# Kernel tuning notes

Hardware: AMD Instinct MI355X
Metric: run time of the kernel (lower is better)

## Reference

```python
import jax, jax.numpy as jnp
import numpy as np

DIM = 172
MULT = 4
HEADS = 1
B, H, W = 2, 256, 256


def _ln(x, g, b):
    # LayerNorm over last dim, eps=1e-5 (torch default)
    m = jnp.mean(x, axis=-1, keepdims=True)
    v = jnp.mean((x - m) ** 2, axis=-1, keepdims=True)
    return (x - m) * jax.lax.rsqrt(v + 1e-5) * g + b


def _l2norm(x):
    # F.normalize(p=2, dim=-1): x / max(||x||, 1e-12)
    n = jnp.sqrt(jnp.sum(x * x, axis=-1, keepdims=True))
    return x / jnp.maximum(n, 1e-12)


def _gelu(x):
    return jax.nn.gelu(x, approximate=False)


def _dwconv3(x, w):
    # x: [B,C,H,W], w: [C,1,3,3], groups=C, padding=1
    return jax.lax.conv_general_dilated(
        x, w, window_strides=(1, 1), padding='SAME',
        feature_group_count=x.shape[1],
        dimension_numbers=('NCHW', 'OIHW', 'NCHW'))


def _c1x1(x, w):
    # 1x1 conv, no bias. x: [B,I,H,W], w: [O,I,1,1]
    return jnp.einsum('bihw,oi->bohw', x, w[:, :, 0, 0])


def _ms_msa(x, Wq, Wk, Wv, rescale, proj_w, proj_b, pos_w1, pos_w2):
    # x: [b,h,w,c] (already layer-normed)
    b, h, w, c = x.shape
    d = c // HEADS
    n = h * w
    xf = x.reshape(b, n, c)
    q_inp = xf @ Wq.T
    k_inp = xf @ Wk.T
    v_inp = xf @ Wv.T

    def split(t):  # -> [b, heads, d, n]  (b n (h d) -> b h n d, then transpose(-2,-1))
        return t.reshape(b, n, HEADS, d).transpose(0, 2, 3, 1)

    q, k, v = split(q_inp), split(k_inp), split(v_inp)
    q = _l2norm(q)
    k = _l2norm(k)
    attn = jnp.einsum('bhdn,bhen->bhde', k, q)  # k @ q^T -> [b,heads,d,d]
    attn = attn * rescale                        # learnable per-head rescale
    attn = jax.nn.softmax(attn, axis=-1)
    xo = jnp.einsum('bhde,bhen->bhdn', attn, v)  # [b,heads,d,n]
    xo = xo.transpose(0, 3, 1, 2).reshape(b, n, HEADS * d)
    out_c = (xo @ proj_w.T + proj_b).reshape(b, h, w, c)
    # residual positional embedding: depthwise conv -> GELU -> depthwise conv on v_inp
    vim = v_inp.reshape(b, h, w, c).transpose(0, 3, 1, 2)
    out_p = _dwconv3(_gelu(_dwconv3(vim, pos_w1)), pos_w2).transpose(0, 2, 3, 1)
    return out_c + out_p


def _ffn(x, w1, dw, w2):
    # FeedForward: 1x1 expand -> GELU -> 3x3 depthwise -> GELU -> 1x1 project
    y = x.transpose(0, 3, 1, 2)
    y = _gelu(_c1x1(y, w1))
    y = _gelu(_dwconv3(y, dw))
    y = _c1x1(y, w2)
    return y.transpose(0, 2, 3, 1)


def reference(x, ln1_g, ln1_b, Wq, Wk, Wv, rescale, proj_w, proj_b,
              pos_w1, pos_w2, ln2_g, ln2_b, ff_w1, ff_dw, ff_w2):
    # SMSAB forward, num_blocks=1. x: [b,c,h,w]
    y = x.transpose(0, 2, 3, 1)  # [b,h,w,c]
    y = _ms_msa(_ln(y, ln1_g, ln1_b), Wq, Wk, Wv, rescale,
                proj_w, proj_b, pos_w1, pos_w2) + y
    y = _ffn(_ln(y, ln2_g, ln2_b), ff_w1, ff_dw, ff_w2) + y
    return y.transpose(0, 3, 1, 2)  # [b,c,h,w]


def setup_inputs() -> dict:
    key = jax.random.key(0)
    ks = jax.random.split(key, 9)
    s = 0.02
    c, m = DIM, DIM * MULT
    return {
        'x': jax.random.normal(ks[0], (B, c, H, W), jnp.float32),
        'ln1_g': jnp.ones((c,), jnp.float32),
        'ln1_b': jnp.zeros((c,), jnp.float32),
        'Wq': jax.random.normal(ks[1], (c, c), jnp.float32) * s,
        'Wk': jax.random.normal(ks[2], (c, c), jnp.float32) * s,
        'Wv': jax.random.normal(ks[3], (c, c), jnp.float32) * s,
        'rescale': jnp.ones((HEADS, 1, 1), jnp.float32),
        'proj_w': jax.random.normal(ks[4], (c, c), jnp.float32) * s,
        'proj_b': jnp.zeros((c,), jnp.float32),
        'pos_w1': jax.random.normal(ks[5], (c, 1, 3, 3), jnp.float32) * s,
        'pos_w2': jax.random.normal(ks[6], (c, 1, 3, 3), jnp.float32) * s,
        'ln2_g': jnp.ones((c,), jnp.float32),
        'ln2_b': jnp.zeros((c,), jnp.float32),
        'ff_w1': jax.random.normal(ks[7], (m, c, 1, 1), jnp.float32) * s,
        'ff_dw': jax.random.normal(ks[8], (m, 1, 3, 3), jnp.float32) * s,
        'ff_w2': jax.random.normal(jax.random.fold_in(key, 99), (c, m, 1, 1), jnp.float32) * s,
    }
```

## Files before the change

kernel.cpp:

```cpp
#include <hip/hip_runtime.h>
#include <hip/hip_bf16.h>
#include <hip/hip_fp16.h>

#define NPIX 65536
#define CP 176
#define EP 704
#define HCC 32

typedef long long i64;
typedef __attribute__((ext_vector_type(8))) short bf8v;
typedef __attribute__((ext_vector_type(8))) float f8v;
typedef __attribute__((ext_vector_type(4))) float f4v;

__device__ __forceinline__ float b2f(unsigned short u) {
  return __uint_as_float(((unsigned)u) << 16);
}
__device__ __forceinline__ short f2b(float v) {
  __hip_bfloat16 h = __float2bfloat16(v);
  return *reinterpret_cast<short*>(&h);
}
__device__ __forceinline__ float ldf(const void* p, i64 i, int bf) {
  return bf ? b2f(((const unsigned short*)p)[i]) : ((const float*)p)[i];
}
__device__ __forceinline__ float gelu_f(float x) {
  return x / (1.f + __expf(-1.702f * x));
}
__device__ __forceinline__ bf8v ldbf8(const short* p) { return *(const bf8v*)p; }

__global__ void detect_k(const void* g, int* flag) {
  unsigned u = *(const unsigned*)g;
  *flag = (u == 0x3F800000u) ? 0 : 1;
}

__global__ __launch_bounds__(256) void prep_k(
    const void* Wv, const void* fw1, const void* fw2, const void* Wq,
    const void* posw1, const void* posw2, const void* fdw,
    const void* pb, const void* ln2g, const void* ln2b,
    short* Wvb, short* fw1b, short* fw2b, float* Wqt,
    float* p1f, float* p2f, float* fdwf, float* pbf, float* gf, float* bfv,
    float* Gf, const int* flagp)
{
  const int flag = *flagp;
  const int bx = blockIdx.x, t = threadIdx.x;
  switch (blockIdx.y) {
    case 0: {
      if (t < 176) Wvb[(i64)bx * 176 + t] =
        f2b((bx < 172 && t < 172) ? ldf(Wv, (i64)bx * 172 + t, flag) : 0.f);
    } break;
    case 1: {
      if (t < 176)
        for (int m = bx; m < 704; m += 176)
          fw1b[(i64)m * 176 + t] =
            f2b((m < 688 && t < 172) ? ldf(fw1, (i64)m * 172 + t, flag) : 0.f);
    } break;
    case 2: {
      for (int k = t; k < 704; k += 256)
        fw2b[(i64)bx * 704 + k] =
          f2b((bx < 172 && k < 688) ? ldf(fw2, (i64)bx * 688 + k, flag) : 0.f);
    } break;
    case 3: {
      if (t < 176) Wqt[(i64)bx * 176 + t] =
        (bx < 172 && t < 172) ? ldf(Wq, (i64)t * 172 + bx, flag) : 0.f;
    } break;
    case 4: {
      if (bx < 9 && t < 176) p1f[bx * 176 + t] = (t < 172) ? ldf(posw1, (i64)t * 9 + bx, flag) : 0.f;
    } break;
    case 5: {
      if (bx < 9 && t < 176) p2f[bx * 176 + t] = (t < 172) ? ldf(posw2, (i64)t * 9 + bx, flag) : 0.f;
    } break;
    case 6: {
      if (bx < 9)
        for (int c = t; c < 704; c += 256)
          fdwf[bx * 704 + c] = (c < 688) ? ldf(fdw, (i64)c * 9 + bx, flag) : 0.f;
    } break;
    case 7: {
      if (bx == 0 && t < 176) {
        pbf[t] = (t < 172) ? ldf(pb, t, flag) : 0.f;
        gf[t]  = (t < 172) ? ldf(ln2g, t, flag) : 0.f;
        bfv[t] = (t < 172) ? ldf(ln2b, t, flag) : 0.f;
      }
    } break;
    default: {
      for (int i = bx * 256 + t; i < 2 * 176 * 176; i += 176 * 256) Gf[i] = 0.f;
    } break;
  }
}

__global__ __launch_bounds__(256) void ln1_k(const void* __restrict__ x,
    const void* __restrict__ g, const void* __restrict__ bv,
    short* __restrict__ A1, const int* __restrict__ flagp)
{
  const int flag = *flagp;
  __shared__ float gs[176], bs[176];
  __shared__ float part[64][9];
  const int tid = threadIdx.x;
  if (tid < 176) {
    gs[tid] = (tid < 172) ? ldf(g, tid, flag) : 0.f;
    bs[tid] = (tid < 172) ? ldf(bv, tid, flag) : 0.f;
  }
  const int w = tid >> 6, l = tid & 63;
  const i64 gp = (i64)blockIdx.x * 64 + l;
  const int b = (int)(gp >> 16); const i64 n = gp & 65535;
  const i64 xb = (i64)b * 172 * NPIX + n;
  const bf8v z = {0, 0, 0, 0, 0, 0, 0, 0};
  bf8v keep[6];
  float s = 0.f, s2 = 0.f;
  #pragma unroll
  for (int i = 0; i < 6; ++i) {
    int c8 = w + i * 4;
    bf8v t = z;
    if (c8 < 22) {
      #pragma unroll
      for (int j = 0; j < 8; ++j) {
        int c = c8 * 8 + j;
        float v = 0.f;
        if (c < 172) { v = ldf(x, xb + (i64)c * NPIX, flag); s += v; s2 += v * v; }
        t[j] = f2b(v);
      }
    }
    keep[i] = t;
  }
  part[l][w * 2] = s; part[l][w * 2 + 1] = s2;
  __syncthreads();
  float S  = part[l][0] + part[l][2] + part[l][4] + part[l][6];
  float S2 = part[l][1] + part[l][3] + part[l][5] + part[l][7];
  float m = S * (1.f / 172.f);
  float rstd = rsqrtf(S2 * (1.f / 172.f) - m * m + 1e-5f);
  #pragma unroll
  for (int i = 0; i < 6; ++i) {
    int c8 = w + i * 4;
    if (c8 < 22) {
      bf8v t = keep[i], o;
      #pragma unroll
      for (int j = 0; j < 8; ++j) {
        int c = c8 * 8 + j;
        float y = (c < 172) ? (b2f((unsigned short)t[j]) - m) * rstd * gs[c] + bs[c] : 0.f;
        o[j] = f2b(y);
      }
      *(bf8v*)(A1 + gp * 176 + c8 * 8) = o;
    }
  }
}

__global__ __launch_bounds__(256) void gg_k(const short* __restrict__ A1,
                                            float* __restrict__ Gf)
{
  __shared__ short tile[176 * 136];
  const int tid = threadIdx.x;
  const int w = tid >> 6, l = tid & 63, lm = l & 15, ld = l >> 4;
  const int b = blockIdx.y;
  const int row = tid & 127, h = tid >> 7;
  const bf8v z = {0, 0, 0, 0, 0, 0, 0, 0};

  f4v acc[3][11];
  #pragma unroll
  for (int i = 0; i < 3; ++i)
    #pragma unroll
    for (int f = 0; f < 11; ++f) acc[i][f] = f4v{0.f, 0.f, 0.f, 0.f};

  for (int sub = 0; sub < 4; ++sub) {
    __syncthreads();
    const i64 nbase = (i64)blockIdx.x * 512 + sub * 128;
    const short* src = A1 + ((i64)b * NPIX + nbase + row) * 176 + h * 88;
    #pragma unroll
    for (int i = 0; i < 11; ++i) {
      bf8v v = ldbf8(src + i * 8);
      int c0 = h * 88 + i * 8;
      #pragma unroll
      for (int j = 0; j < 8; ++j) tile[(c0 + j) * 136 + row] = v[j];
    }
    __syncthreads();
    #pragma unroll
    for (int ks = 0; ks < 4; ++ks) {
      const int ko = ks * 32 + ld * 8;
      bf8v av[3], bv[11];
      #pragma unroll
      for (int i = 0; i < 3; ++i) {
        int fd = w + i * 4;
        av[i] = (fd < 11) ? *(const bf8v*)&tile[(fd * 16 + lm) * 136 + ko] : z;
      }
      #pragma unroll
      for (int f = 0; f < 11; ++f)
        bv[f] = *(const bf8v*)&tile[(f * 16 + lm) * 136 + ko];
      #pragma unroll
      for (int i = 0; i < 3; ++i)
        #pragma unroll
        for (int f = 0; f < 11; ++f)
          acc[i][f] = __builtin_amdgcn_mfma_f32_16x16x32_bf16(av[i], bv[f], acc[i][f], 0, 0, 0);
    }
  }
  #pragma unroll
  for (int i = 0; i < 3; ++i) {
    int fd = w + i * 4;
    if (fd >= 11) continue;
    #pragma unroll
    for (int f = 0; f < 11; ++f)
      #pragma unroll
      for (int r = 0; r < 4; ++r) {
        int d = fd * 16 + ld * 4 + r;
        int e = f * 16 + lm;
        atomicAdd(Gf + ((i64)b * 176 + d) * 176 + e, acc[i][f][r]);
      }
  }
}

__global__ __launch_bounds__(256) void attn_k1(const float* __restrict__ Gf,
    const void* __restrict__ Wk, const void* __restrict__ Wq,
    float* __restrict__ T, float* __restrict__ invk, float* __restrict__ invq,
    const int* __restrict__ flagp)
{
  const int flag = *flagp;
  const int d = blockIdx.x, b = blockIdx.y, e = threadIdx.x;
  const float* G = Gf + (i64)b * 176 * 176;
  float t = 0.f, tq = 0.f;
  if (e < 176) {
    for (int c = 0; c < 172; ++c) {
      float g = G[(i64)c * 176 + e];
      t  += ldf(Wk, (i64)d * 172 + c, flag) * g;
      tq += ldf(Wq, (i64)d * 172 + c, flag) * g;
    }
    T[((i64)b * 176 + d) * 176 + e] = t;
  }
  float pk = (e < 172) ? t  * ldf(Wk, (i64)d * 172 + e, flag) : 0.f;
  float pq = (e < 172) ? tq * ldf(Wq, (i64)d * 172 + e, flag) : 0.f;
  __shared__ float r1[256], r2[256];
  r1[e] = pk; r2[e] = pq; __syncthreads();
  for (int st = 128; st > 0; st >>= 1) {
    if (e < st) { r1[e] += r1[e + st]; r2[e] += r2[e + st]; }
    __syncthreads();
  }
  if (e == 0) {
    invk[b * 176 + d] = 1.f / fmaxf(sqrtf(fmaxf(r1[0], 0.f)), 1e-12f);
    invq[b * 176 + d] = 1.f / fmaxf(sqrtf(fmaxf(r2[0], 0.f)), 1e-12f);
  }
}

__global__ __launch_bounds__(256) void attn_k2(const float* __restrict__ T,
    const float* __restrict__ Wqt, const float* __restrict__ invk,
    const float* __restrict__ invq, const void* __restrict__ resc,
    float* __restrict__ attnf, const int* __restrict__ flagp)
{
  const int flag = *flagp;
  const int d = blockIdx.x, b = blockIdx.y, e = threadIdx.x;
  __shared__ float tl[176];
  const float* Trow = T + ((i64)b * 176 + d) * 176;
  if (e < 176) tl[e] = Trow[e];
  __syncthreads();
  float val = -1e30f;
  if (e < 172) {
    float a = 0.f;
    for (int c = 0; c < 172; ++c) a += tl[c] * Wqt[(i64)c * 176 + e];
    val = a * invk[b * 176 + d] * invq[b * 176 + e] * ldf(resc, 0, flag);
  }
  __shared__ float red[256];
  red[e] = val; __syncthreads();
  for (int st = 128; st > 0; st >>= 1) {
    if (e < st) red[e] = fmaxf(red[e], red[e + st]);
    __syncthreads();
  }
  float mx = red[0]; __syncthreads();
  float ex = (e < 172) ? __expf(val - mx) : 0.f;
  red[e] = ex; __syncthreads();
  for (int st = 128; st > 0; st >>= 1) {
    if (e < st) red[e] += red[e + st];
    __syncthreads();
  }
  float sm = red[0];
  if (e < 176) attnf[((i64)b * 176 + d) * 176 + e] = (e < 172) ? ex / sm : 0.f;
}

__global__ __launch_bounds__(256) void attn_k3(const float* __restrict__ attnf,
    const void* __restrict__ pw, short* __restrict__ Mb, const int* __restrict__ flagp)
{
  const int flag = *flagp;
  const int o = blockIdx.x, b = blockIdx.y, e = threadIdx.x;
  if (e >= 176) return;
  float m = 0.f;
  if (o < 172 && e < 172)
    for (int d = 0; d < 172; ++d)
      m += ldf(pw, (i64)o * 172 + d, flag) * attnf[((i64)b * 176 + d) * 176 + e];
  Mb[((i64)b * CP + o) * CP + e] = f2b(m);
}

__global__ __launch_bounds__(256) void ffn1_k(
    const short* __restrict__ A1,
    const short* __restrict__ fw1b,
    const float* __restrict__ fdwf,
    short* __restrict__ F, i64 fbs,
    int y0glob)
{
  __shared__ __half ering[3][256][HCC];
  __shared__ __half2 wl[9][HCC / 2];
  const int tid = threadIdx.x;
  const int w = tid >> 6, l = tid & 63, lm = l & 15, ld = l >> 4;
  const int hc0 = blockIdx.x * HCC;
  const int b = blockIdx.z;
  const int yb0 = y0glob + blockIdx.y * 8;
  for (int i = tid; i < 9 * HCC; i += 256)
    ((__half*)wl)[i] = __float2half(fdwf[(i / HCC) * EP + hc0 + (i % HCC)]);

  const short* Wl = fw1b + (i64)(hc0 + lm) * CP + ld * 8;
  const bf8v z = {0, 0, 0, 0, 0, 0, 0, 0};

  for (int yy = yb0 - 1; yy <= yb0 + 8; ++yy) {
    const int slot = (yy - (yb0 - 1)) % 3;
    __syncthreads();
    if (yy >= 0 && yy < 256) {
      const i64 prow = (i64)b * NPIX + (i64)yy * 256;
      const short* Xbase = A1 + prow * CP;
      f4v acc[2][4];
      #pragma unroll
      for (int m = 0; m < 2; ++m)
        #pragma unroll
        for (int nt = 0; nt < 4; ++nt) acc[m][nt] = f4v{0.f, 0.f, 0.f, 0.f};
      #pragma unroll
      for (int ks = 0; ks < 6; ++ks) {
        const int ko = ks * 32;
        const bool ok = (ks < 5) || (ld < 2);
        bf8v av[4], bv[2];
        #pragma unroll
        for (int nt = 0; nt < 4; ++nt) {
          const int px0 = (w * 4 + nt) * 16;
          av[nt] = ok ? ldbf8(Xbase + (i64)(px0 + lm) * CP + ld * 8 + ko) : z;
        }
        #pragma unroll
        for (int m = 0; m < 2; ++m)
          bv[m] = ok ? ldbf8(Wl + (i64)m * 16 * CP + ko) : z;
        #pragma unroll
        for (int m = 0; m < 2; ++m)
          #pragma unroll
          for (int nt = 0; nt < 4; ++nt)
            acc[m][nt] = __builtin_amdgcn_mfma_f32_16x16x32_bf16(av[nt], bv[m], acc[m][nt], 0, 0, 0);
      }
      #pragma unroll
      for (int m = 0; m < 2; ++m)
        #pragma unroll
        for (int nt = 0; nt < 4; ++nt) {
          const int px0 = (w * 4 + nt) * 16;
          #pragma unroll
          for (int r = 0; r < 4; ++r)
            ering[slot][px0 + ld * 4 + r][m * 16 + lm] = __float2half(gelu_f(acc[m][nt][r]));
        }
    } else {
      unsigned* ep = (unsigned*)&ering[slot][0][0];
      for (int i = tid; i < 256 * HCC / 2; i += 256) ep[i] = 0u;
    }
    __syncthreads();
    const int fy = yy - 1;
    if (fy >= yb0 && fy <= yb0 + 7) {
      #pragma unroll
      for (int it = 0; it < 4; ++it) {
        const int item = tid + it * 256;
        const int px = item >> 2, g = item & 3;
        __half2 a4[4];
        #pragma unroll
        for (int j = 0; j < 4; ++j) a4[j] = __half2{__half(0.f), __half(0.f)};
        #pragma unroll
        for (int dy = -1; dy <= 1; ++dy) {
          const int sl = (fy + dy - yb0 + 1) % 3;
          #pragma unroll
          for (int dx = -1; dx <= 1; ++dx) {
            const int xx = px + dx;
            if (xx < 0 || xx > 255) continue;
            const __half2* v = (const __half2*)&ering[sl][xx][g * 8];
            const __half2* wp = &wl[(dy + 1) * 3 + (dx + 1)][g * 4];
            #pragma unroll
            for (int j = 0; j < 4; ++j) a4[j] = __hfma2(v[j], wp[j], a4[j]);
          }
        }
        bf8v o;
        #pragma unroll
        for (int j = 0; j < 4; ++j) {
          float2 f = __half22float2(a4[j]);
          o[2 * j]     = f2b(gelu_f(f.x));
          o[2 * j + 1] = f2b(gelu_f(f.y));
        }
        const i64 frow = (i64)(fy - y0glob) * 256 + px;
        *(bf8v*)(F + b * fbs + frow * (i64)EP + hc0 + g * 8) = o;
      }
    }
  }
}

template<int MODE, bool GELU_>
__global__ __launch_bounds__(256) void gemm_k(
    const short* __restrict__ Wb, i64 wbs,
    const short* __restrict__ X, i64 xbs, int Kp,
    const float* __restrict__ bias,
    const short* __restrict__ add0, i64 a0bs,
    const void* __restrict__ xres,
    void* __restrict__ outp, i64 obs, int ocols, i64 out_n0,
    short* __restrict__ Y1,
    const float* __restrict__ gf, const float* __restrict__ bfv,
    const int* __restrict__ flagp)
{
  __shared__ short tl[(MODE >= 2) ? 4 * 32 * 176 : 1];
  __shared__ float2 stt[(MODE == 3) ? 4 * 32 : 1];
  const int tid = threadIdx.x;
  const int w = tid >> 6, l = tid & 63;
  const int lm = l & 15, ld = l >> 4;
  const int b = blockIdx.z;
  const int co0 = blockIdx.y * CP;
  const i64 nloc = (i64)blockIdx.x * 128 + w * 32;

  const short* Xl = X + b * xbs + (nloc + lm) * (i64)Kp + ld * 8;
  const short* Wl = Wb + b * wbs + (i64)(co0 + lm) * Kp + ld * 8;

  f4v acc[2][11];
  #pragma unroll
  for (int a = 0; a < 2; ++a)
    #pragma unroll
    for (int f = 0; f < 11; ++f) acc[a][f] = f4v{0.f, 0.f, 0.f, 0.f};

  const int nfull = Kp >> 5;
  for (int s = 0; s < nfull; ++s) {
    const int ko = s * 32;
    bf8v av0 = ldbf8(Xl + ko);
    bf8v av1 = ldbf8(Xl + (i64)16 * Kp + ko);
    bf8v bv[11];
    #pragma unroll
    for (int f = 0; f < 11; ++f) bv[f] = ldbf8(Wl + (i64)f * 16 * Kp + ko);
    #pragma unroll
    for (int f = 0; f < 11; ++f) {
      acc[0][f] = __builtin_amdgcn_mfma_f32_16x16x32_bf16(av0, bv[f], acc[0][f], 0, 0, 0);
      acc[1][f] = __builtin_amdgcn_mfma_f32_16x16x32_bf16(av1, bv[f], acc[1][f], 0, 0, 0);
    }
  }
  if (Kp & 31) {
    const int ko = nfull * 32;
    const bf8v z = {0, 0, 0, 0, 0, 0, 0, 0};
    const bool ok = (ld < 2);
    bf8v av0 = ok ? ldbf8(Xl + ko) : z;
    bf8v av1 = ok ? ldbf8(Xl + (i64)16 * Kp + ko) : z;
    bf8v bv[11];
    #pragma unroll
    for (int f = 0; f < 11; ++f) bv[f] = ok ? ldbf8(Wl + (i64)f * 16 * Kp + ko) : z;
    #pragma unroll
    for (int f = 0; f < 11; ++f) {
      acc[0][f] = __builtin_amdgcn_mfma_f32_16x16x32_bf16(av0, bv[f], acc[0][f], 0, 0, 0);
      acc[1][f] = __builtin_amdgcn_mfma_f32_16x16x32_bf16(av1, bv[f], acc[1][f], 0, 0, 0);
    }
  }

  const int flag = (MODE >= 2) ? *flagp : 0;

  if (MODE == 0) {
    #pragma unroll
    for (int a = 0; a < 2; ++a)
      #pragma unroll
      for (int f = 0; f < 11; ++f) {
        const int col = co0 + f * 16 + lm;
        #pragma unroll
        for (int r = 0; r < 4; ++r) {
          float v = acc[a][f][r];
          if (GELU_) v = gelu_f(v);
          const i64 row = nloc + a * 16 + ld * 4 + r;
          ((short*)outp)[b * obs + row * ocols + col] = f2b(v);
        }
      }
  } else if (MODE == 2) {
    #pragma unroll
    for (int a = 0; a < 2; ++a)
      #pragma unroll
      for (int f = 0; f < 11; ++f) {
        const int col = co0 + f * 16 + lm;
        #pragma unroll
        for (int r = 0; r < 4; ++r) {
          const int row32 = a * 16 + ld * 4 + r;
          tl[(w * 32 + row32) * 176 + col] = f2b(acc[a][f][r]);
        }
      }
    #pragma unroll
    for (int cc = 0; cc < 3; ++cc) {
      const int col = l + cc * 64;
      if (col < 172) {
        const i64 gn = out_n0 + nloc;
        bf8v vv[4], yv[4];
        #pragma unroll
        for (int i = 0; i < 4; ++i)
          #pragma unroll
          for (int j = 0; j < 8; ++j)
            vv[i][j] = tl[(w * 32 + i * 8 + j) * 176 + col];
        const short* yp = Y1 + ((i64)b * CP + col) * NPIX + gn;
        #pragma unroll
        for (int i = 0; i < 4; ++i) yv[i] = ldbf8(yp + i * 8);
        if (flag) {
          short* op = (short*)outp + ((i64)b * 172 + col) * NPIX + gn;
          #pragma unroll
          for (int i = 0; i < 4; ++i) {
            bf8v ov;
            #pragma unroll
            for (int j = 0; j < 8; ++j)
              ov[j] = f2b(b2f((unsigned short)vv[i][j]) + b2f((unsigned short)yv[i][j]));
            *(bf8v*)(op + i * 8) = ov;
          }
        } else {
          float* op = (float*)outp + ((i64)b * 172 + col) * NPIX + gn;
          #pragma unroll
          for (int i = 0; i < 4; ++i) {
            f8v fo;
            #pragma unroll
            for (int j = 0; j < 8; ++j)
              fo[j] = b2f((unsigned short)vv[i][j]) + b2f((unsigned short)yv[i][j]);
            *(f8v*)(op + i * 8) = fo;
          }
        }
      }
    }
  } else {
    #pragma unroll
    for (int a = 0; a < 2; ++a)
      #pragma unroll
      for (int f = 0; f < 11; ++f) {
        const int col = co0 + f * 16 + lm;
        const float bvl = bias ? bias[col] : 0.f;
        #pragma unroll
        for (int r = 0; r < 4; ++r) {
          float v = acc[a][f][r] + bvl;
          const int row32 = a * 16 + ld * 4 + r;
          const i64 row = nloc + row32;
          v += b2f(((const unsigned short*)add0)[b * a0bs + row * ocols + col]);
          tl[(w * 32 + row32) * 176 + col] = f2b(v);
        }
      }
    #pragma unroll
    for (int cc = 0; cc < 3; ++cc) {
      const int col = l + cc * 64;
      if (col < 172) {
        bf8v vv[4];
        #pragma unroll
        for (int i = 0; i < 4; ++i)
          #pragma unroll
          for (int j = 0; j < 8; ++j)
            vv[i][j] = tl[(w * 32 + i * 8 + j) * 176 + col];
        const i64 xoff = ((i64)b * 172 + col) * NPIX + nloc;
        if (flag) {
          #pragma unroll
          for (int i = 0; i < 4; ++i) {
            bf8v xv = ldbf8((const short*)xres + xoff + i * 8);
            #pragma unroll
            for (int j = 0; j < 8; ++j)
              vv[i][j] = f2b(b2f((unsigned short)vv[i][j]) + b2f((unsigned short)xv[j]));
          }
        } else {
          const float* xp = (const float*)xres + xoff;
          #pragma unroll
          for (int i = 0; i < 4; ++i) {
            f8v xv = *(const f8v*)(xp + i * 8);
            #pragma unroll
            for (int j = 0; j < 8; ++j)
              vv[i][j] = f2b(b2f((unsigned short)vv[i][j]) + xv[j]);
          }
        }
        short* yp = Y1 + ((i64)b * CP + col) * NPIX + nloc;
        #pragma unroll
        for (int i = 0; i < 4; ++i) {
          #pragma unroll
          for (int j = 0; j < 8; ++j)
            tl[(w * 32 + i * 8 + j) * 176 + col] = vv[i][j];
          *(bf8v*)(yp + i * 8) = vv[i];
        }
      }
    }
    {
      const int p = l >> 1, h = l & 1;
      float s_ = 0.f, q_ = 0.f;
      #pragma unroll
      for (int ii = 0; ii < 11; ++ii) {
        bf8v v = *(const bf8v*)&tl[(w * 32 + p) * 176 + (h * 11 + ii) * 8];
        #pragma unroll
        for (int j = 0; j < 8; ++j) { float t = b2f((unsigned short)v[j]); s_ += t; q_ += t * t; }
      }
      s_ += __shfl_xor(s_, 1); q_ += __shfl_xor(q_, 1);
      if (h == 0) {
        float mean = s_ * (1.f / 172.f);
        float rstd = rsqrtf(q_ * (1.f / 172.f) - mean * mean + 1e-5f);
        stt[w * 32 + p] = make_float2(mean, rstd);
      }
    }
    #pragma unroll
    for (int ii = 0; ii < 11; ++ii) {
      const int ch = l + ii * 64;
      const int p = ch / 22, g = ch % 22;
      float2 st = stt[w * 32 + p];
      f8v gv = *(const f8v*)(gf + g * 8);
      f8v bv2 = *(const f8v*)(bfv + g * 8);
      bf8v v = *(const bf8v*)&tl[(w * 32 + p) * 176 + g * 8];
      bf8v o;
      #pragma unroll
      for (int j = 0; j < 8; ++j)
        o[j] = f2b((b2f((unsigned short)v[j]) - st.x) * st.y * gv[j] + bv2[j]);
      *(bf8v*)((short*)outp + b * obs + (nloc + p) * (i64)ocols + g * 8) = o;
    }
  }
}

template<int RC, bool GELU_>
__global__ __launch_bounds__(256) void dwc_k(const short* __restrict__ in, i64 ibs,
    int iy0, const float* __restrict__ wf,
    short* __restrict__ out, i64 obs, int oy0)
{
  constexpr int Cp = RC * 8;
  __shared__ float wl[9 * Cp];
  for (int i = threadIdx.x; i < 9 * Cp; i += 256) wl[i] = wf[i];
  __syncthreads();
  const int b = blockIdx.z;
  const int yl = blockIdx.y;
  const int yg = oy0 + yl;
  const int cir = blockIdx.x * 256 + threadIdx.x;
  const int x = cir / RC, g = cir % RC;
  float acc[8] = {0.f, 0.f, 0.f, 0.f, 0.f, 0.f, 0.f, 0.f};
  #pragma unroll
  for (int dy = -1; dy <= 1; ++dy) {
    const int yy = yg + dy;
    if (yy < 0 || yy > 255) continue;
    const short* rp = in + b * ibs + (i64)(yy - iy0) * (256 * RC) * 8;
    #pragma unroll
    for (int dx = -1; dx <= 1; ++dx) {
      const int xx = x + dx;
      if (xx < 0 || xx > 255) continue;
      bf8v v = ldbf8(rp + (i64)(cir + dx * RC) * 8);
      const float* wp = wl + ((dy + 1) * 3 + (dx + 1)) * Cp + g * 8;
      #pragma unroll
      for (int j = 0; j < 8; ++j) acc[j] += b2f((unsigned short)v[j]) * wp[j];
    }
  }
  bf8v o;
  #pragma unroll
  for (int j = 0; j < 8; ++j) o[j] = f2b(GELU_ ? gelu_f(acc[j]) : acc[j]);
  *(bf8v*)(out + b * obs + ((i64)yl * (256 * RC) + cir) * 8) = o;
}

extern "C" void kernel_launch(void* const* d_in, const int* in_sizes, int n_in,
                              void* d_out, int out_size, void* d_ws, size_t ws_size,
                              hipStream_t stream)
{
  const void* x     = d_in[0];
  const void* ln1g  = d_in[1];
  const void* ln1b  = d_in[2];
  const void* Wq    = d_in[3];
  const void* Wk    = d_in[4];
  const void* Wv    = d_in[5];
  const void* resc  = d_in[6];
  const void* pw    = d_in[7];
  const void* pb    = d_in[8];
  const void* posw1 = d_in[9];
  const void* posw2 = d_in[10];
  const void* ln2g  = d_in[11];
  const void* ln2b  = d_in[12];
  const void* fw1   = d_in[13];
  const void* fdw   = d_in[14];
  const void* fw2   = d_in[15];

  char* ws = (char*)d_ws;
  size_t off = 0;
  auto alloc = [&](size_t bytes) {
    void* p = ws + off;
    off = (off + bytes + 255) & ~(size_t)255;
    return p;
  };
  int*    flagp = (int*)   alloc(16);
  float*  invq  = (float*) alloc(2 * 176 * 4);
  float*  invk  = (float*) alloc(2 * 176 * 4);
  float*  Gf    = (float*) alloc((size_t)2 * 176 * 176 * 4);
  float*  Tf    = (float*) alloc((size_t)2 * 176 * 176 * 4);
  float*  attnf = (float*) alloc((size_t)2 * 176 * 176 * 4);
  short*  Mb    = (short*) alloc((size_t)2 * CP * CP * 2);
  float*  Wqt   = (float*) alloc((size_t)176 * 176 * 4);
  short*  Wvb   = (short*) alloc((size_t)CP * CP * 2);
  short*  fw1b  = (short*) alloc((size_t)EP * CP * 2);
  short*  fw2b  = (short*) alloc((size_t)CP * EP * 2);
  float*  p1f   = (float*) alloc((size_t)9 * CP * 4);
  float*  p2f   = (float*) alloc((size_t)9 * CP * 4);
  float*  fdwf  = (float*) alloc((size_t)9 * EP * 4);
  float*  pbf   = (float*) alloc((size_t)CP * 4);
  float*  gf    = (float*) alloc((size_t)CP * 4);
  float*  bfv   = (float*) alloc((size_t)CP * 4);
  const size_t BUF = (size_t)2 * NPIX * CP * 2;
  short* A1 = (short*)alloc(BUF);
  short* Yb = (short*)alloc(BUF);
  short* D  = (short*)alloc(BUF);
  short* P2 = (short*)alloc(BUF);
  alloc(4 * 1024 * 1024);
  if (off > ws_size) return;

  const i64 CBS  = (i64)NPIX * CP;
  const i64 FBS2 = (i64)32768 * EP;
  short* F = D;

  detect_k<<<1, 1, 0, stream>>>(ln1g, flagp);

  prep_k<<<dim3(176, 9), 256, 0, stream>>>(Wv, fw1, fw2, Wq, posw1, posw2, fdw,
      pb, ln2g, ln2b, Wvb, fw1b, fw2b, Wqt, p1f, p2f, fdwf, pbf, gf, bfv,
      Gf, flagp);

  ln1_k<<<2048, 256, 0, stream>>>(x, ln1g, ln1b, A1, flagp);

  gg_k<<<dim3(128, 2), 256, 0, stream>>>(A1, Gf);
  attn_k1<<<dim3(172, 2), 256, 0, stream>>>(Gf, Wk, Wq, Tf, invk, invq, flagp);
  attn_k2<<<dim3(172, 2), 256, 0, stream>>>(Tf, Wqt, invk, invq, resc, attnf, flagp);
  attn_k3<<<dim3(176, 2), 256, 0, stream>>>(attnf, pw, Mb, flagp);

  gemm_k<0, false><<<dim3(512, 1, 2), 256, 0, stream>>>(
      Wvb, 0, A1, CBS, CP, nullptr, nullptr, 0, nullptr,
      D, CBS, CP, 0, nullptr, nullptr, nullptr, flagp);

  dwc_k<22, true ><<<dim3(22, 256, 2), 256, 0, stream>>>(D,  CBS, 0, p1f, Yb, CBS, 0);
  dwc_k<22, false><<<dim3(22, 256, 2), 256, 0, stream>>>(Yb, CBS, 0, p2f, P2, CBS, 0);

  gemm_k<3, false><<<dim3(512, 1, 2), 256, 0, stream>>>(
      Mb, (i64)CP * CP, D, CBS, CP, pbf, P2, CBS, x,
      A1, CBS, CP, 0, Yb, gf, bfv, flagp);

  for (int ci = 0; ci < 2; ++ci) {
    ffn1_k<<<dim3(22, 16, 2), 256, 0, stream>>>(
        A1, fw1b, fdwf, F, FBS2, ci * 128);
    gemm_k<2, false><<<dim3(256, 1, 2), 256, 0, stream>>>(
        fw2b, 0, F, FBS2, EP, nullptr, nullptr, 0, nullptr,
        d_out, 0, 0, (i64)ci * 32768, Yb, nullptr, nullptr, flagp);
  }
}
```

Baseline: 803.3 us.

## Compute FFN depthwise GELU in fp16 with register-blocked stencil and fp16 projection

The fused FFN expand+depthwise kernel now has each thread compute four adjacent pixels. It loads a 6-pixel window of each ring row into registers once and reuses it across the three horizontal taps, which cuts LDS reads. The final GELU is evaluated in packed half2 arithmetic instead of converting to float, and the intermediate F is stored as fp16 rather than bf16. The second FFN projection weights are converted to fp16 and that GEMM mode switches to the f16 MFMA. This removes the float conversions and redundant shared-memory loads, at the cost of fp16 range/precision risk in GELU and the accumulated activations.

```diff
diff --git a/kernel.cpp b/kernel.cpp
--- a/kernel.cpp
+++ b/kernel.cpp
@@ -9,6 +9,7 @@
 
 typedef long long i64;
 typedef __attribute__((ext_vector_type(8))) short bf8v;
+typedef __attribute__((ext_vector_type(8))) _Float16 h8v;
 typedef __attribute__((ext_vector_type(8))) float f8v;
 typedef __attribute__((ext_vector_type(4))) float f4v;
 
@@ -24,6 +25,10 @@
 }
 __device__ __forceinline__ float gelu_f(float x) {
   return x / (1.f + __expf(-1.702f * x));
+}
+__device__ __forceinline__ __half2 gelu_h2(__half2 x) {
+  __half2 e = h2exp(__hmul2(x, __float2half2_rn(-1.702f)));
+  return __hmul2(x, h2rcp(__hadd2(__float2half2_rn(1.f), e)));
 }
 __device__ __forceinline__ bf8v ldbf8(const short* p) { return *(const bf8v*)p; }
 
@@ -54,9 +59,11 @@
             f2b((m < 688 && t < 172) ? ldf(fw1, (i64)m * 172 + t, flag) : 0.f);
     } break;
     case 2: {
-      for (int k = t; k < 704; k += 256)
-        fw2b[(i64)bx * 704 + k] =
-          f2b((bx < 172 && k < 688) ? ldf(fw2, (i64)bx * 688 + k, flag) : 0.f);
+      for (int k = t; k < 704; k += 256) {
+        float v = (bx < 172 && k < 688) ? ldf(fw2, (i64)bx * 688 + k, flag) : 0.f;
+        __half h = __float2half(v);
+        fw2b[(i64)bx * 704 + k] = *reinterpret_cast<short*>(&h);
+      }
     } break;
     case 3: {
       if (t < 176) Wqt[(i64)bx * 176 + t] =
@@ -301,6 +308,7 @@
 
   const short* Wl = fw1b + (i64)(hc0 + lm) * CP + ld * 8;
   const bf8v z = {0, 0, 0, 0, 0, 0, 0, 0};
+  const __half2 zh2 = __float2half2_rn(0.f);
 
   for (int yy = yb0 - 1; yy <= yb0 + 8; ++yy) {
     const int slot = (yy - (yb0 - 1)) % 3;
@@ -348,35 +356,46 @@
     __syncthreads();
     const int fy = yy - 1;
     if (fy >= yb0 && fy <= yb0 + 7) {
-      #pragma unroll
-      for (int it = 0; it < 4; ++it) {
-        const int item = tid + it * 256;
-        const int px = item >> 2, g = item & 3;
-        __half2 a4[4];
-        #pragma unroll
-        for (int j = 0; j < 4; ++j) a4[j] = __half2{__half(0.f), __half(0.f)};
-        #pragma unroll
-        for (int dy = -1; dy <= 1; ++dy) {
-          const int sl = (fy + dy - yb0 + 1) % 3;
-          #pragma unroll
-          for (int dx = -1; dx <= 1; ++dx) {
-            const int xx = px + dx;
-            if (xx < 0 || xx > 255) continue;
+      const int pq = tid >> 2, g = tid & 3;
+      const int px0 = pq * 4;
+      __half2 acc2[4][4];
+      #pragma unroll
+      for (int p = 0; p < 4; ++p)
+        #pragma unroll
+        for (int j = 0; j < 4; ++j) acc2[p][j] = zh2;
+      #pragma unroll
+      for (int dy = 0; dy < 3; ++dy) {
+        const int sl = (fy + dy - yb0) % 3;
+        __half2 vbuf[6][4];
+        #pragma unroll
+        for (int i = 0; i < 6; ++i) {
+          const int xx = px0 - 1 + i;
+          if (xx < 0 || xx > 255) {
+            #pragma unroll
+            for (int j = 0; j < 4; ++j) vbuf[i][j] = zh2;
+          } else {
             const __half2* v = (const __half2*)&ering[sl][xx][g * 8];
-            const __half2* wp = &wl[(dy + 1) * 3 + (dx + 1)][g * 4];
             #pragma unroll
-            for (int j = 0; j < 4; ++j) a4[j] = __hfma2(v[j], wp[j], a4[j]);
+            for (int j = 0; j < 4; ++j) vbuf[i][j] = v[j];
           }
         }
-        bf8v o;
-        #pragma unroll
-        for (int j = 0; j < 4; ++j) {
-          float2 f = __half22float2(a4[j]);
-          o[2 * j]     = f2b(gelu_f(f.x));
-          o[2 * j + 1] = f2b(gelu_f(f.y));
-        }
-        const i64 frow = (i64)(fy - y0glob) * 256 + px;
-        *(bf8v*)(F + b * fbs + frow * (i64)EP + hc0 + g * 8) = o;
+        #pragma unroll
+        for (int dx = 0; dx < 3; ++dx) {
+          const __half2* wp = &wl[dy * 3 + dx][g * 4];
+          #pragma unroll
+          for (int p = 0; p < 4; ++p)
+            #pragma unroll
+            for (int j = 0; j < 4; ++j)
+              acc2[p][j] = __hfma2(vbuf[p + dx][j], wp[j], acc2[p][j]);
+        }
+      }
+      #pragma unroll
+      for (int p = 0; p < 4; ++p) {
+        union { __half2 h[4]; bf8v v; } u;
+        #pragma unroll
+        for (int j = 0; j < 4; ++j) u.h[j] = gelu_h2(acc2[p][j]);
+        const i64 frow = (i64)(fy - y0glob) * 256 + px0 + p;
+        *(bf8v*)(F + b * fbs + frow * (i64)EP + hc0 + g * 8) = u.v;
       }
     }
   }
@@ -422,8 +441,15 @@
     for (int f = 0; f < 11; ++f) bv[f] = ldbf8(Wl + (i64)f * 16 * Kp + ko);
     #pragma unroll
     for (int f = 0; f < 11; ++f) {
-      acc[0][f] = __builtin_amdgcn_mfma_f32_16x16x32_bf16(av0, bv[f], acc[0][f], 0, 0, 0);
-      acc[1][f] = __builtin_amdgcn_mfma_f32_16x16x32_bf16(av1, bv[f], acc[1][f], 0, 0, 0);
+      if (MODE == 2) {
+        acc[0][f] = __builtin_amdgcn_mfma_f32_16x16x32_f16(
+            __builtin_bit_cast(h8v, av0), __builtin_bit_cast(h8v, bv[f]), acc[0][f], 0, 0, 0);
+        acc[1][f] = __builtin_amdgcn_mfma_f32_16x16x32_f16(
+            __builtin_bit_cast(h8v, av1), __builtin_bit_cast(h8v, bv[f]), acc[1][f], 0, 0, 0);
+      } else {
+        acc[0][f] = __builtin_amdgcn_mfma_f32_16x16x32_bf16(av0, bv[f], acc[0][f], 0, 0, 0);
+        acc[1][f] = __builtin_amdgcn_mfma_f32_16x16x32_bf16(av1, bv[f], acc[1][f], 0, 0, 0);
+      }
     }
   }
   if (Kp & 31) {
@@ -437,8 +463,15 @@
     for (int f = 0; f < 11; ++f) bv[f] = ok ? ldbf8(Wl + (i64)f * 16 * Kp + ko) : z;
     #pragma unroll
     for (int f = 0; f < 11; ++f) {
-      acc[0][f] = __builtin_amdgcn_mfma_f32_16x16x32_bf16(av0, bv[f], acc[0][f], 0, 0, 0);
-      acc[1][f] = __builtin_amdgcn_mfma_f32_16x16x32_bf16(av1, bv[f], acc[1][f], 0, 0, 0);
+      if (MODE == 2) {
+        acc[0][f] = __builtin_amdgcn_mfma_f32_16x16x32_f16(
+            __builtin_bit_cast(h8v, av0), __builtin_bit_cast(h8v, bv[f]), acc[0][f], 0, 0, 0);
+        acc[1][f] = __builtin_amdgcn_mfma_f32_16x16x32_f16(
+            __builtin_bit_cast(h8v, av1), __builtin_bit_cast(h8v, bv[f]), acc[1][f], 0, 0, 0);
+      } else {
+        acc[0][f] = __builtin_amdgcn_mfma_f32_16x16x32_bf16(av0, bv[f], acc[0][f], 0, 0, 0);
+        acc[1][f] = __builtin_amdgcn_mfma_f32_16x16x32_bf16(av1, bv[f], acc[1][f], 0, 0, 0);
+      }
     }
   }
 
```

After: 828.6 us. +3.1%, slower.
